# Optimization experiments

Hardware: AMD Instinct MI355X
Metric: run time of the kernel (lower is better)

Reference implementation:

```python
import jax, jax.numpy as jnp
import numpy as np

B, N, C, H = 8, 4096, 256, 8
D = C // H
HID = 4 * C
EPS = 1e-5

def _ln(x, w, b):
    mu = jnp.mean(x, axis=-1, keepdims=True)
    var = jnp.var(x, axis=-1, keepdims=True)
    return (x - mu) * jax.lax.rsqrt(var + EPS) * w + b

def setup_inputs() -> dict:
    key = jax.random.key(0)
    ks = jax.random.split(key, 16)
    s = lambda k, shp, scale=0.02: jax.random.normal(k, shp, dtype=jnp.float32) * scale
    return {
        "input_": jax.random.normal(ks[0], (B, N, C), dtype=jnp.float32),
        "prev_state": jax.random.normal(ks[1], (B, N, C), dtype=jnp.float32),
        "pos_embed": jax.random.normal(ks[2], (1, N, C), dtype=jnp.float32),
        "norm1_w": jnp.ones((C,), jnp.float32), "norm1_b": jnp.zeros((C,), jnp.float32),
        "norm2_w": jnp.ones((C,), jnp.float32), "norm2_b": jnp.zeros((C,), jnp.float32),
        "norm3_w": jnp.ones((C,), jnp.float32), "norm3_b": jnp.zeros((C,), jnp.float32),
        "qkv_input_w": s(ks[3], (3 * C, C)),
        "qkv_state_w": s(ks[4], (3 * C, C)),
        "proj_w": s(ks[5], (C, C)), "proj_b": jnp.zeros((C,), jnp.float32),
        "gate_w": s(ks[6], (C, 2 * C)), "gate_b": jnp.zeros((C,), jnp.float32),
        "fc1_w": s(ks[7], (HID, C)), "fc1_b": jnp.zeros((HID,), jnp.float32),
        "fc2_w": s(ks[8], (C, HID)), "fc2_b": jnp.zeros((C,), jnp.float32),
    }

def reference(input_, prev_state, pos_embed,
              norm1_w, norm1_b, norm2_w, norm2_b, norm3_w, norm3_b,
              qkv_input_w, qkv_state_w, proj_w, proj_b,
              gate_w, gate_b, fc1_w, fc1_b, fc2_w, fc2_b):
    input_pos = input_ + pos_embed
    x_ln = _ln(input_pos, norm1_w, norm1_b)
    s_ln = _ln(prev_state, norm2_w, norm2_b)
    # fused QKV from input and state; torch Linear: x @ W.T
    qkv_i = (x_ln @ qkv_input_w.T).reshape(B, N, 3, H, D).transpose(2, 0, 3, 1, 4)
    qkv_s = (s_ln @ qkv_state_w.T).reshape(B, N, 3, H, D).transpose(2, 0, 3, 1, 4)
    q = qkv_i[0] + qkv_s[0]  # [B,H,N,D]
    k = qkv_i[1] + qkv_s[1]
    v = qkv_i[2] + qkv_s[2]
    phi_q = jax.nn.elu(q) + 1.0
    phi_k = jax.nn.elu(k) + 1.0
    # (phi_q @ phi_k^T) @ v reordered associatively to O(N*D^2)
    kv = jnp.einsum('bhnd,bhne->bhde', phi_k, v)        # [B,H,D,D]
    attn = jnp.einsum('bhnd,bhde->bhne', phi_q, kv)     # [B,H,N,D]
    attn = attn.transpose(0, 2, 1, 3).reshape(B, N, C)
    attn = attn @ proj_w.T + proj_b
    output = input_pos + attn
    stacked = jnp.concatenate([input_, prev_state], axis=2)
    update = jax.nn.sigmoid(stacked @ gate_w.T + gate_b)
    new_state = prev_state * (1.0 - update) + attn * update
    h = _ln(output, norm3_w, norm3_b)
    h = jax.nn.gelu(h @ fc1_w.T + fc1_b, approximate=False) @ fc2_w.T + fc2_b
    output = output + h
    return (output, new_state)
```

## Files before the change

### kernel.cpp

```cpp
#include <hip/hip_runtime.h>
#include <cmath>

typedef unsigned short u16;
typedef __attribute__((ext_vector_type(8))) short short8;
typedef __attribute__((ext_vector_type(4))) float f32x4;
typedef __attribute__((ext_vector_type(4))) u16 u16x4;

__device__ __forceinline__ float b2f(u16 u) {
    unsigned x = ((unsigned)u) << 16;
    return __builtin_bit_cast(float, x);
}
__device__ __forceinline__ u16 f2b(float f) {
    unsigned x = __builtin_bit_cast(unsigned, f);
    unsigned r = (x + 0x7fffu + ((x >> 16) & 1u)) >> 16;
    return (u16)r;
}
__device__ __forceinline__ float loadx(const void* p, size_t i, int f32) {
    return f32 ? ((const float*)p)[i] : b2f(((const u16*)p)[i]);
}
__device__ __forceinline__ void gl_lds16(const void* g, void* l) {
    __builtin_amdgcn_global_load_lds(
        (const __attribute__((address_space(1))) void*)g,
        (__attribute__((address_space(3))) void*)l, 16, 0, 0);
}
__device__ __forceinline__ float gelu_f(float x) {
    float y = 0.7978845608028654f * (x + 0.044715f * x * x * x);
    float e = __expf(2.f * y);
    float t = 1.f - 2.f / (e + 1.f);
    return 0.5f * x * (1.f + t);
}

#define BB 8
#define NN 4096
#define CC 256
#define HH 8
#define DD 32
#define HID 1024
#define MTOK (BB*NN)
#define TOKEL ((size_t)MTOK*CC)
#define TOKELC 8388608

#define WS_INPUT_POS 0u
#define WS_PHIQ   16777216u
#define WS_PHIK   33554432u
#define WS_V      50331648u
#define WS_XLN    67108864u
#define WS_SLN    83886080u
#define WS_OUTPRE 100663296u
#define WS_FLAG   117440512u

#define OFF_QKVI  0u
#define OFF_QKVS  196608u
#define OFF_PROJW 393216u
#define OFF_GATEW 458752u
#define OFF_FC1W  589824u
#define OFF_FC2W  851968u
#define OFF_PROJB 1114112u
#define OFF_GATEB 1114368u
#define OFF_FC1B  1114624u
#define OFF_FC2B  1115648u
#define WTOT      1115904u

__device__ __attribute__((aligned(16))) u16 g_wb[WTOT];
__device__ __attribute__((aligned(16))) u16 g_inb[TOKELC];
__device__ __attribute__((aligned(16))) u16 g_prevb[TOKELC];

__global__ __launch_bounds__(64) void detect_kernel(const u16* __restrict__ in0,
                                                    int* __restrict__ flag)
{
    int t = threadIdx.x;
    u16 w = in0[2 * t];
    int e = (w >> 7) & 0xFF;
    int bad = (e < 64 || e > 192) ? 1 : 0;
    unsigned long long m = __ballot(bad);
    if (t == 0) *flag = (__popcll(m) > 8) ? 1 : 0;
}

__global__ __launch_bounds__(256) void wconv_kernel(
    const void* qkvi, const void* qkvs, const void* projw, const void* gatew,
    const void* fc1w, const void* fc2w, const void* projb, const void* gateb,
    const void* fc1b, const void* fc2b, const int* __restrict__ flagp)
{
    const int f32 = *flagp;
    unsigned i = blockIdx.x * 256 + threadIdx.x;
    if (i >= WTOT) return;
    const void* src; unsigned off;
    if      (i < OFF_QKVS)  { src = qkvi;  off = OFF_QKVI; }
    else if (i < OFF_PROJW) { src = qkvs;  off = OFF_QKVS; }
    else if (i < OFF_GATEW) { src = projw; off = OFF_PROJW; }
    else if (i < OFF_FC1W)  { src = gatew; off = OFF_GATEW; }
    else if (i < OFF_FC2W)  { src = fc1w;  off = OFF_FC1W; }
    else if (i < OFF_PROJB) { src = fc2w;  off = OFF_FC2W; }
    else if (i < OFF_GATEB) { src = projb; off = OFF_PROJB; }
    else if (i < OFF_FC1B)  { src = gateb; off = OFF_GATEB; }
    else if (i < OFF_FC2B)  { src = fc1b;  off = OFF_FC1B; }
    else                    { src = fc2b;  off = OFF_FC2B; }
    g_wb[i] = f2b(loadx(src, i - off, f32));
}

__global__ __launch_bounds__(256) void prep_kernel(
    const void* __restrict__ inp, const void* __restrict__ prev,
    const void* __restrict__ pos,
    const void* __restrict__ w1, const void* __restrict__ b1,
    const void* __restrict__ w2, const void* __restrict__ b2,
    u16* __restrict__ input_pos, u16* __restrict__ x_ln, u16* __restrict__ s_ln,
    const int* __restrict__ flagp)
{
    const int f32 = *flagp;
    const int m = blockIdx.x;
    const int c = threadIdx.x;
    const int n = m & (NN - 1);
    const size_t idx = (size_t)m * CC + c;

    __shared__ float red[8];

    float inr = loadx(inp, idx, f32);
    float ip = inr + loadx(pos, (size_t)n * CC + c, f32);
    g_inb[idx] = f2b(inr);
    float s = ip, s2 = ip * ip;
    #pragma unroll
    for (int o = 32; o; o >>= 1) { s += __shfl_down(s, o, 64); s2 += __shfl_down(s2, o, 64); }
    if ((threadIdx.x & 63) == 0) { int w6 = threadIdx.x >> 6; red[w6] = s; red[4 + w6] = s2; }
    __syncthreads();
    float mu  = (red[0] + red[1] + red[2] + red[3]) * (1.f / 256.f);
    float var = (red[4] + red[5] + red[6] + red[7]) * (1.f / 256.f) - mu * mu;
    float rs = rsqrtf(var + 1e-5f);
    input_pos[idx] = f2b(ip);
    x_ln[idx] = f2b((ip - mu) * rs * loadx(w1, c, f32) + loadx(b1, c, f32));
    __syncthreads();

    float pv = loadx(prev, idx, f32);
    g_prevb[idx] = f2b(pv);
    s = pv; s2 = pv * pv;
    #pragma unroll
    for (int o = 32; o; o >>= 1) { s += __shfl_down(s, o, 64); s2 += __shfl_down(s2, o, 64); }
    if ((threadIdx.x & 63) == 0) { int w6 = threadIdx.x >> 6; red[w6] = s; red[4 + w6] = s2; }
    __syncthreads();
    mu  = (red[0] + red[1] + red[2] + red[3]) * (1.f / 256.f);
    var = (red[4] + red[5] + red[6] + red[7]) * (1.f / 256.f) - mu * mu;
    rs = rsqrtf(var + 1e-5f);
    s_ln[idx] = f2b((pv - mu) * rs * loadx(w2, c, f32) + loadx(b2, c, f32));
}

__global__ __launch_bounds__(256) void ln3_kernel(
    const u16* __restrict__ op, const void* __restrict__ w,
    const void* __restrict__ b, u16* __restrict__ out, const int* __restrict__ flagp)
{
    const int f32 = *flagp;
    const size_t m = blockIdx.x;
    const int c = threadIdx.x;
    const size_t idx = m * CC + c;
    __shared__ float red[8];
    float x = b2f(op[idx]);
    float s = x, s2 = x * x;
    #pragma unroll
    for (int o = 32; o; o >>= 1) { s += __shfl_down(s, o, 64); s2 += __shfl_down(s2, o, 64); }
    if ((threadIdx.x & 63) == 0) { int w6 = threadIdx.x >> 6; red[w6] = s; red[4 + w6] = s2; }
    __syncthreads();
    float mu  = (red[0] + red[1] + red[2] + red[3]) * (1.f / 256.f);
    float var = (red[4] + red[5] + red[6] + red[7]) * (1.f / 256.f) - mu * mu;
    out[idx] = f2b((x - mu) * rsqrtf(var + 1e-5f) * loadx(w, c, f32) + loadx(b, c, f32));
}

__global__ __launch_bounds__(64) void kv_mfma(
    const u16* __restrict__ phik_t, const u16* __restrict__ v_t,
    float* __restrict__ kvout)
{
    const int bh = blockIdx.x;
    const int k0 = blockIdx.y * 256;
    const int lane = threadIdx.x;
    const int quad = lane >> 4, lr = lane & 15;

    const u16* A = phik_t + (size_t)bh * DD * NN;
    const u16* W = v_t    + (size_t)bh * DD * NN;

    f32x4 acc[2][2];
    #pragma unroll
    for (int i = 0; i < 2; ++i)
        #pragma unroll
        for (int j = 0; j < 2; ++j) { f32x4 z = {0.f,0.f,0.f,0.f}; acc[i][j] = z; }

    for (int kk = k0; kk < k0 + 256; kk += 32) {
        short8 a0 = *(const short8*)(A + (size_t)lr * NN + kk + quad * 8);
        short8 a1 = *(const short8*)(A + (size_t)(16 + lr) * NN + kk + quad * 8);
        short8 w0 = *(const short8*)(W + (size_t)lr * NN + kk + quad * 8);
        short8 w1 = *(const short8*)(W + (size_t)(16 + lr) * NN + kk + quad * 8);
        acc[0][0] = __builtin_amdgcn_mfma_f32_16x16x32_bf16(a0, w0, acc[0][0], 0, 0, 0);
        acc[0][1] = __builtin_amdgcn_mfma_f32_16x16x32_bf16(a0, w1, acc[0][1], 0, 0, 0);
        acc[1][0] = __builtin_amdgcn_mfma_f32_16x16x32_bf16(a1, w0, acc[1][0], 0, 0, 0);
        acc[1][1] = __builtin_amdgcn_mfma_f32_16x16x32_bf16(a1, w1, acc[1][1], 0, 0, 0);
    }
    float* base = kvout + (size_t)bh * (DD * DD);
    #pragma unroll
    for (int i = 0; i < 2; ++i)
        #pragma unroll
        for (int j = 0; j < 2; ++j)
            #pragma unroll
            for (int r = 0; r < 4; ++r)
                atomicAdd(base + (i * 16 + quad * 4 + r) * DD + j * 16 + lr, acc[i][j][r]);
}

__global__ __launch_bounds__(256) void attn_mfma(
    const u16* __restrict__ phiq, const float* __restrict__ kv,
    u16* __restrict__ attn_tok)
{
    const int bh = blockIdx.x;
    const int b = bh >> 3, h = bh & 7;
    const int wv = threadIdx.x >> 6, lane = threadIdx.x & 63;
    const int quad = lane >> 4, lr = lane & 15;

    const float* kvb = kv + (size_t)bh * (DD * DD);
    short8 bf0, bf1;
    #pragma unroll
    for (int j = 0; j < 8; ++j) {
        int d = quad * 8 + j;
        bf0[j] = (short)f2b(kvb[d * DD + lr]);
        bf1[j] = (short)f2b(kvb[d * DD + 16 + lr]);
    }

    const u16* qb = phiq + (size_t)bh * NN * DD;
    const int n0 = blockIdx.y * 512 + wv * 128;
    #pragma unroll
    for (int t = 0; t < 8; ++t) {
        const int nt = n0 + t * 16;
        short8 af = *(const short8*)(qb + (size_t)(nt + lr) * DD + quad * 8);
        f32x4 c0 = {0.f,0.f,0.f,0.f}, c1 = {0.f,0.f,0.f,0.f};
        c0 = __builtin_amdgcn_mfma_f32_16x16x32_bf16(af, bf0, c0, 0, 0, 0);
        c1 = __builtin_amdgcn_mfma_f32_16x16x32_bf16(af, bf1, c1, 0, 0, 0);
        size_t base = ((size_t)b * NN + nt + quad * 4) * CC + h * DD;
        #pragma unroll
        for (int r = 0; r < 4; ++r) {
            attn_tok[base + (size_t)r * CC + lr]      = f2b(c0[r]);
            attn_tok[base + (size_t)r * CC + 16 + lr] = f2b(c1[r]);
        }
    }
}

#define BM 128
#define BN 128
#define BK 32

template <int MODE>
__global__ __launch_bounds__(256) void gemm_bt(
    const u16* __restrict__ A1in, const u16* __restrict__ A2in,
    int lda, int ldw, int K, int Ksplit, int wcol2,
    u16* __restrict__ o0, u16* __restrict__ o1,
    const u16* __restrict__ xa, const void* __restrict__ xr,
    void* __restrict__ oraw, const int* __restrict__ flagp)
{
    __shared__ __attribute__((aligned(16))) u16 ash[3][BM * BK];
    __shared__ __attribute__((aligned(16))) u16 bsh[3][BN * BK];

    const int f32 = (MODE == 2 || MODE == 4) ? *flagp : 0;

    const u16* W1; const u16* W2; const u16* bias = nullptr;
    if (MODE == 0)      { W1 = g_wb + OFF_QKVI; W2 = g_wb + OFF_QKVS; }
    else if (MODE == 1) { W1 = W2 = g_wb + OFF_PROJW; bias = g_wb + OFF_PROJB; }
    else if (MODE == 2) { W1 = W2 = g_wb + OFF_GATEW; bias = g_wb + OFF_GATEB; }
    else if (MODE == 3) { W1 = W2 = g_wb + OFF_FC1W;  bias = g_wb + OFF_FC1B; }
    else                { W1 = W2 = g_wb + OFF_FC2W;  bias = g_wb + OFF_FC2B; }
    const u16* A1 = (MODE == 2) ? g_inb   : A1in;
    const u16* A2 = (MODE == 2) ? g_prevb : A2in;

    const int gx = gridDim.x;
    const int nwg = gx * (int)gridDim.y;
    const int hw = blockIdx.y * gx + blockIdx.x;
    const int qq = nwg >> 3, rr = nwg & 7;
    const int xc = hw & 7, pp = hw >> 3;
    const int nid = (xc < rr ? xc * (qq + 1) : rr * (qq + 1) + (xc - rr) * qq) + pp;
    const int bx = nid % gx, by = nid / gx;

    const int tid = threadIdx.x;
    const int lane = tid & 63;
    const int wv = tid >> 6;
    const int wm = wv >> 1, wn = wv & 1;
    const int quad = lane >> 4, lr = lane & 15;

    const bool swp = (MODE == 0) ? (bx < 2) : true;

    f32x4 acc[4][4];
    #pragma unroll
    for (int i = 0; i < 4; ++i)
        #pragma unroll
        for (int j = 0; j < 4; ++j) { f32x4 z = {0.f,0.f,0.f,0.f}; acc[i][j] = z; }

    const size_t arow0 = (size_t)by * BM;
    const size_t wrow0 = (size_t)bx * BN;

    const int srow = lane & 31;
    const int sg   = (lane >> 5) << 3;
    const size_t aoff = (arow0 + wv * 32 + srow) * (size_t)lda + sg;
    const size_t woff = (wrow0 + wv * 32 + srow) * (size_t)ldw + sg;

    auto stage = [&](int buf, int k0) {
        const u16* As; const u16* Ws; int ka, kw;
        if (k0 < Ksplit) { As = A1; Ws = W1; ka = k0;          kw = k0; }
        else             { As = A2; Ws = W2; ka = k0 - Ksplit; kw = k0 - Ksplit + wcol2; }
        const u16* ga = As + aoff + ka;
        u16* la = ash[buf] + (wv << 10);
        gl_lds16(ga, la);
        gl_lds16(ga + 16, la + 512);
        const u16* gw = Ws + woff + kw;
        u16* lb = bsh[buf] + (wv << 10);
        gl_lds16(gw, lb);
        gl_lds16(gw + 16, lb + 512);
    };

    auto compute = [&](int buf) {
        short8 af[4], bf[4];
        #pragma unroll
        for (int i = 0; i < 4; ++i) {
            const int ra = wm * 64 + i * 16 + lr;
            af[i] = *(const short8*)(ash[buf] + ((ra >> 5) << 10) + (quad << 8) + ((ra & 31) << 3));
        }
        #pragma unroll
        for (int j = 0; j < 4; ++j) {
            const int rb = wn * 64 + j * 16 + lr;
            bf[j] = *(const short8*)(bsh[buf] + ((rb >> 5) << 10) + (quad << 8) + ((rb & 31) << 3));
        }
        if (swp) {
            #pragma unroll
            for (int i = 0; i < 4; ++i)
                #pragma unroll
                for (int j = 0; j < 4; ++j)
                    acc[i][j] = __builtin_amdgcn_mfma_f32_16x16x32_bf16(bf[j], af[i], acc[i][j], 0, 0, 0);
        } else {
            #pragma unroll
            for (int i = 0; i < 4; ++i)
                #pragma unroll
                for (int j = 0; j < 4; ++j)
                    acc[i][j] = __builtin_amdgcn_mfma_f32_16x16x32_bf16(af[i], bf[j], acc[i][j], 0, 0, 0);
        }
    };

    const int NT = K / BK;
    stage(0, 0);
    stage(1, BK);
    for (int t = 0; t < NT; ++t) {
        if (t + 2 < NT) {
            stage((t + 2) % 3, (t + 2) * BK);
            asm volatile("s_waitcnt vmcnt(8)" ::: "memory");
        } else if (t + 1 < NT) {
            asm volatile("s_waitcnt vmcnt(4)" ::: "memory");
        } else {
            asm volatile("s_waitcnt vmcnt(0)" ::: "memory");
        }
        __builtin_amdgcn_s_barrier();
        asm volatile("" ::: "memory");
        compute(t % 3);
        asm volatile("" ::: "memory");
        __builtin_amdgcn_s_barrier();
    }

    const int mbase = by * BM + wm * 64;
    const int nbase = bx * BN + wn * 64;
    constexpr int LDOUT = (MODE == 3) ? HID : CC;

    #pragma unroll
    for (int i = 0; i < 4; ++i) {
        #pragma unroll
        for (int j = 0; j < 4; ++j) {
            if (MODE == 0) {
                if (swp) {
                    const int m = mbase + i * 16 + lr;
                    const int b = m >> 12, n = m & (NN - 1);
                    const int c0 = nbase + j * 16 + quad * 4;
                    const int h = c0 >> 5, d0 = c0 & 31;
                    u16x4 p;
                    #pragma unroll
                    for (int r = 0; r < 4; ++r) {
                        float v = acc[i][j][r];
                        p[r] = f2b((v > 0.f) ? (v + 1.f) : __expf(v));
                    }
                    *(u16x4*)(o0 + (((size_t)b * HH + h) * NN + n) * DD + d0) = p;
                } else {
                    const int c = nbase + j * 16 + lr;
                    const int which = c >> 8, rem = c & 255, h = rem >> 5, d = rem & 31;
                    const int m0 = mbase + i * 16 + quad * 4;
                    const int b = m0 >> 12, n0i = m0 & (NN - 1);
                    u16x4 p;
                    #pragma unroll
                    for (int r = 0; r < 4; ++r) {
                        float v = acc[i][j][r];
                        if (which == 1) v = (v > 0.f) ? (v + 1.f) : __expf(v);
                        p[r] = f2b(v);
                    }
                    u16* dst = o0 + (size_t)which * TOKEL;
                    *(u16x4*)(dst + (((size_t)b * HH + h) * DD + d) * NN + n0i) = p;
                }
            } else {
                const int m = mbase + i * 16 + lr;
                const int c0 = nbase + j * 16 + quad * 4;
                const size_t idx0 = (size_t)m * LDOUT + c0;
                float bias4[4];
                {
                    u16x4 t = *(const u16x4*)(bias + c0);
                    #pragma unroll
                    for (int r = 0; r < 4; ++r) bias4[r] = b2f(t[r]);
                }
                if (MODE == 1) {
                    u16x4 xa4 = *(const u16x4*)(xa + idx0);
                    u16x4 po, pr;
                    #pragma unroll
                    for (int r = 0; r < 4; ++r) {
                        float val = acc[i][j][r] + bias4[r];
                        po[r] = f2b(val);
                        pr[r] = f2b(b2f(xa4[r]) + val);
                    }
                    *(u16x4*)(o0 + idx0) = po;
                    *(u16x4*)(o1 + idx0) = pr;
                } else if (MODE == 2) {
                    u16x4 ap4 = *(const u16x4*)(xa + idx0);
                    if (f32) {
                        f32x4 pv = *(const f32x4*)((const float*)xr + idx0);
                        f32x4 o;
                        #pragma unroll
                        for (int r = 0; r < 4; ++r) {
                            float u = 1.f / (1.f + __expf(-(acc[i][j][r] + bias4[r])));
                            o[r] = pv[r] * (1.f - u) + b2f(ap4[r]) * u;
                        }
                        *(f32x4*)((float*)oraw + TOKEL + idx0) = o;
                    } else {
                        u16x4 pv = *(const u16x4*)((const u16*)xr + idx0);
                        u16x4 o;
                        #pragma unroll
                        for (int r = 0; r < 4; ++r) {
                            float u = 1.f / (1.f + __expf(-(acc[i][j][r] + bias4[r])));
                            o[r] = f2b(b2f(pv[r]) * (1.f - u) + b2f(ap4[r]) * u);
                        }
                        *(u16x4*)((u16*)oraw + TOKEL + idx0) = o;
                    }
                } else if (MODE == 3) {
                    u16x4 p;
                    #pragma unroll
                    for (int r = 0; r < 4; ++r)
                        p[r] = f2b(gelu_f(acc[i][j][r] + bias4[r]));
                    *(u16x4*)(o0 + idx0) = p;
                } else {
                    u16x4 xa4 = *(const u16x4*)(xa + idx0);
                    if (f32) {
                        f32x4 o;
                        #pragma unroll
                        for (int r = 0; r < 4; ++r)
                            o[r] = b2f(xa4[r]) + acc[i][j][r] + bias4[r];
                        *(f32x4*)((float*)oraw + idx0) = o;
                    } else {
                        u16x4 o;
                        #pragma unroll
                        for (int r = 0; r < 4; ++r)
                            o[r] = f2b(b2f(xa4[r]) + acc[i][j][r] + bias4[r]);
                        *(u16x4*)((u16*)oraw + idx0) = o;
                    }
                }
            }
        }
    }
}

extern "C" void kernel_launch(void* const* d_in, const int* in_sizes, int n_in,
                              void* d_out, int out_size, void* d_ws, size_t ws_size,
                              hipStream_t stream)
{
    const void* input_ = d_in[0];
    const void* prev   = d_in[1];
    const void* pos    = d_in[2];
    const void* n1w = d_in[3];  const void* n1b = d_in[4];
    const void* n2w = d_in[5];  const void* n2b = d_in[6];
    const void* n3w = d_in[7];  const void* n3b = d_in[8];
    const void* qkvi = d_in[9]; const void* qkvs = d_in[10];
    const void* projw = d_in[11]; const void* projb = d_in[12];
    const void* gatew = d_in[13]; const void* gateb = d_in[14];
    const void* fc1w = d_in[15]; const void* fc1b = d_in[16];
    const void* fc2w = d_in[17]; const void* fc2b = d_in[18];

    char* ws = (char*)d_ws;
    u16* input_pos = (u16*)(ws + WS_INPUT_POS);
    u16* phiq  = (u16*)(ws + WS_PHIQ);
    u16* phikt = (u16*)(ws + WS_PHIK);
    u16* vt    = (u16*)(ws + WS_V);
    u16* x_ln = (u16*)(ws + WS_XLN);
    u16* s_ln = (u16*)(ws + WS_SLN);
    u16* attn_tok = x_ln;
    u16* attn_proj = phikt;
    float* kvf = (float*)(ws + WS_SLN);
    u16* ln3o = s_ln;
    u16* outpre = (u16*)(ws + WS_OUTPRE);
    u16* h1 = (u16*)(ws + WS_INPUT_POS);
    int* flagp = (int*)(ws + WS_FLAG);

    detect_kernel<<<1, 64, 0, stream>>>((const u16*)input_, flagp);
    wconv_kernel<<<(WTOT + 255) / 256, 256, 0, stream>>>(
        qkvi, qkvs, projw, gatew, fc1w, fc2w, projb, gateb, fc1b, fc2b, flagp);
    prep_kernel<<<MTOK, 256, 0, stream>>>(input_, prev, pos, n1w, n1b, n2w, n2b,
                                          input_pos, x_ln, s_ln, flagp);
    gemm_bt<0><<<dim3(3 * CC / BN, MTOK / BM), 256, 0, stream>>>(
        x_ln, s_ln, CC, CC, 2 * CC, CC, 0,
        phiq, nullptr, nullptr, nullptr, nullptr, flagp);
    hipMemsetAsync((void*)kvf, 0, BB * HH * DD * DD * sizeof(float), stream);
    kv_mfma<<<dim3(BB * HH, 16), 64, 0, stream>>>(phikt, vt, kvf);
    attn_mfma<<<dim3(BB * HH, NN / 512), 256, 0, stream>>>(phiq, kvf, attn_tok);
    gemm_bt<1><<<dim3(CC / BN, MTOK / BM), 256, 0, stream>>>(
        attn_tok, attn_tok, CC, CC, CC, CC, 0,
        attn_proj, outpre, input_pos, nullptr, nullptr, flagp);
    gemm_bt<2><<<dim3(CC / BN, MTOK / BM), 256, 0, stream>>>(
        nullptr, nullptr, CC, 2 * CC, 2 * CC, CC, CC,
        nullptr, nullptr, attn_proj, prev, d_out, flagp);
    ln3_kernel<<<MTOK, 256, 0, stream>>>(outpre, n3w, n3b, ln3o, flagp);
    gemm_bt<3><<<dim3(HID / BN, MTOK / BM), 256, 0, stream>>>(
        ln3o, ln3o, CC, CC, CC, CC, 0,
        h1, nullptr, nullptr, nullptr, nullptr, flagp);
    gemm_bt<4><<<dim3(CC / BN, MTOK / BM), 256, 0, stream>>>(
        h1, h1, HID, HID, HID, HID, 0,
        nullptr, nullptr, outpre, nullptr, d_out, flagp);
}
```

Baseline: 469.6 us.

## Replace LDS-staged GEMMs with direct-from-global MFMA kernel for proj/gate/fc1/fc2

Result: slower. 535.2 us (+14.0%).

```diff
diff --git a/kernel.cpp b/kernel.cpp
--- a/kernel.cpp
+++ b/kernel.cpp
@@ -236,6 +236,140 @@
     }
 }
 
+template <int MODE>
+__global__ __launch_bounds__(256) void gemm_direct(
+    const u16* __restrict__ A1in, const u16* __restrict__ A2in,
+    int lda, int ldw, int K, int Ksplit, int wcol2,
+    u16* __restrict__ o0, u16* __restrict__ o1,
+    const u16* __restrict__ xa, const void* __restrict__ xr,
+    void* __restrict__ oraw, const int* __restrict__ flagp)
+{
+    const int f32 = (MODE == 2 || MODE == 4) ? *flagp : 0;
+
+    const u16* W1; const u16* W2; const u16* bias;
+    if (MODE == 1)      { W1 = W2 = g_wb + OFF_PROJW; bias = g_wb + OFF_PROJB; }
+    else if (MODE == 2) { W1 = W2 = g_wb + OFF_GATEW; bias = g_wb + OFF_GATEB; }
+    else if (MODE == 3) { W1 = W2 = g_wb + OFF_FC1W;  bias = g_wb + OFF_FC1B; }
+    else                { W1 = W2 = g_wb + OFF_FC2W;  bias = g_wb + OFF_FC2B; }
+    const u16* A1 = (MODE == 2) ? g_inb   : A1in;
+    const u16* A2 = (MODE == 2) ? g_prevb : A2in;
+
+    const int gx = gridDim.x;
+    const int nwg = gx * (int)gridDim.y;
+    const int hw = blockIdx.y * gx + blockIdx.x;
+    const int qq = nwg >> 3, rr = nwg & 7;
+    const int xc = hw & 7, pp = hw >> 3;
+    const int nid = (xc < rr ? xc * (qq + 1) : rr * (qq + 1) + (xc - rr) * qq) + pp;
+    const int bx = nid % gx, by = nid / gx;
+
+    const int lane = threadIdx.x & 63;
+    const int wv = threadIdx.x >> 6;
+    const int quad = lane >> 4, lr = lane & 15;
+
+    const int m0 = by * 256 + wv * 64;
+    const int n0 = bx * 64;
+
+    f32x4 acc[4][4];
+    #pragma unroll
+    for (int i = 0; i < 4; ++i)
+        #pragma unroll
+        for (int j = 0; j < 4; ++j) { f32x4 z = {0.f,0.f,0.f,0.f}; acc[i][j] = z; }
+
+    size_t arow[4], wrow[4];
+    #pragma unroll
+    for (int i = 0; i < 4; ++i) arow[i] = (size_t)(m0 + i * 16 + lr) * lda + quad * 8;
+    #pragma unroll
+    for (int j = 0; j < 4; ++j) wrow[j] = (size_t)(n0 + j * 16 + lr) * ldw + quad * 8;
+
+    #pragma unroll 2
+    for (int k0 = 0; k0 < K; k0 += 32) {
+        const u16* As; const u16* Ws; int ka, kw;
+        if (k0 < Ksplit) { As = A1; Ws = W1; ka = k0;          kw = k0; }
+        else             { As = A2; Ws = W2; ka = k0 - Ksplit; kw = k0 - Ksplit + wcol2; }
+        short8 af[4], bf[4];
+        #pragma unroll
+        for (int i = 0; i < 4; ++i) af[i] = *(const short8*)(As + arow[i] + ka);
+        #pragma unroll
+        for (int j = 0; j < 4; ++j) bf[j] = *(const short8*)(Ws + wrow[j] + kw);
+        #pragma unroll
+        for (int i = 0; i < 4; ++i)
+            #pragma unroll
+            for (int j = 0; j < 4; ++j)
+                acc[i][j] = __builtin_amdgcn_mfma_f32_16x16x32_bf16(bf[j], af[i], acc[i][j], 0, 0, 0);
+    }
+
+    constexpr int LDOUT = (MODE == 3) ? HID : CC;
+    #pragma unroll
+    for (int i = 0; i < 4; ++i) {
+        #pragma unroll
+        for (int j = 0; j < 4; ++j) {
+            const int m = m0 + i * 16 + lr;
+            const int c0 = n0 + j * 16 + quad * 4;
+            const size_t idx0 = (size_t)m * LDOUT + c0;
+            float bias4[4];
+            {
+                u16x4 t = *(const u16x4*)(bias + c0);
+                #pragma unroll
+                for (int r = 0; r < 4; ++r) bias4[r] = b2f(t[r]);
+            }
+            if (MODE == 1) {
+                u16x4 xa4 = *(const u16x4*)(xa + idx0);
+                u16x4 po, pr;
+                #pragma unroll
+                for (int r = 0; r < 4; ++r) {
+                    float val = acc[i][j][r] + bias4[r];
+                    po[r] = f2b(val);
+                    pr[r] = f2b(b2f(xa4[r]) + val);
+                }
+                *(u16x4*)(o0 + idx0) = po;
+                *(u16x4*)(o1 + idx0) = pr;
+            } else if (MODE == 2) {
+                u16x4 ap4 = *(const u16x4*)(xa + idx0);
+                if (f32) {
+                    f32x4 pv = *(const f32x4*)((const float*)xr + idx0);
+                    f32x4 o;
+                    #pragma unroll
+                    for (int r = 0; r < 4; ++r) {
+                        float u = 1.f / (1.f + __expf(-(acc[i][j][r] + bias4[r])));
+                        o[r] = pv[r] * (1.f - u) + b2f(ap4[r]) * u;
+                    }
+                    *(f32x4*)((float*)oraw + TOKEL + idx0) = o;
+                } else {
+                    u16x4 pv = *(const u16x4*)((const u16*)xr + idx0);
+                    u16x4 o;
+                    #pragma unroll
+                    for (int r = 0; r < 4; ++r) {
+                        float u = 1.f / (1.f + __expf(-(acc[i][j][r] + bias4[r])));
+                        o[r] = f2b(b2f(pv[r]) * (1.f - u) + b2f(ap4[r]) * u);
+                    }
+                    *(u16x4*)((u16*)oraw + TOKEL + idx0) = o;
+                }
+            } else if (MODE == 3) {
+                u16x4 p;
+                #pragma unroll
+                for (int r = 0; r < 4; ++r)
+                    p[r] = f2b(gelu_f(acc[i][j][r] + bias4[r]));
+                *(u16x4*)(o0 + idx0) = p;
+            } else {
+                u16x4 xa4 = *(const u16x4*)(xa + idx0);
+                if (f32) {
+                    f32x4 o;
+                    #pragma unroll
+                    for (int r = 0; r < 4; ++r)
+                        o[r] = b2f(xa4[r]) + acc[i][j][r] + bias4[r];
+                    *(f32x4*)((float*)oraw + idx0) = o;
+                } else {
+                    u16x4 o;
+                    #pragma unroll
+                    for (int r = 0; r < 4; ++r)
+                        o[r] = f2b(b2f(xa4[r]) + acc[i][j][r] + bias4[r]);
+                    *(u16x4*)((u16*)oraw + idx0) = o;
+                }
+            }
+        }
+    }
+}
+
 #define BM 128
 #define BN 128
 #define BK 32
@@ -251,16 +385,10 @@
     __shared__ __attribute__((aligned(16))) u16 ash[3][BM * BK];
     __shared__ __attribute__((aligned(16))) u16 bsh[3][BN * BK];
 
-    const int f32 = (MODE == 2 || MODE == 4) ? *flagp : 0;
-
-    const u16* W1; const u16* W2; const u16* bias = nullptr;
-    if (MODE == 0)      { W1 = g_wb + OFF_QKVI; W2 = g_wb + OFF_QKVS; }
-    else if (MODE == 1) { W1 = W2 = g_wb + OFF_PROJW; bias = g_wb + OFF_PROJB; }
-    else if (MODE == 2) { W1 = W2 = g_wb + OFF_GATEW; bias = g_wb + OFF_GATEB; }
-    else if (MODE == 3) { W1 = W2 = g_wb + OFF_FC1W;  bias = g_wb + OFF_FC1B; }
-    else                { W1 = W2 = g_wb + OFF_FC2W;  bias = g_wb + OFF_FC2B; }
-    const u16* A1 = (MODE == 2) ? g_inb   : A1in;
-    const u16* A2 = (MODE == 2) ? g_prevb : A2in;
+    const u16* W1; const u16* W2;
+    W1 = g_wb + OFF_QKVI; W2 = g_wb + OFF_QKVS;
+    const u16* A1 = A1in;
+    const u16* A2 = A2in;
 
     const int gx = gridDim.x;
     const int nwg = gx * (int)gridDim.y;
@@ -276,7 +404,7 @@
     const int wm = wv >> 1, wn = wv & 1;
     const int quad = lane >> 4, lr = lane & 15;
 
-    const bool swp = (MODE == 0) ? (bx < 2) : true;
+    const bool swp = (bx < 2);
 
     f32x4 acc[4][4];
     #pragma unroll
@@ -354,104 +482,37 @@
 
     const int mbase = by * BM + wm * 64;
     const int nbase = bx * BN + wn * 64;
-    constexpr int LDOUT = (MODE == 3) ? HID : CC;
 
     #pragma unroll
     for (int i = 0; i < 4; ++i) {
         #pragma unroll
         for (int j = 0; j < 4; ++j) {
-            if (MODE == 0) {
-                if (swp) {
-                    const int m = mbase + i * 16 + lr;
-                    const int b = m >> 12, n = m & (NN - 1);
-                    const int c0 = nbase + j * 16 + quad * 4;
-                    const int h = c0 >> 5, d0 = c0 & 31;
-                    u16x4 p;
-                    #pragma unroll
-                    for (int r = 0; r < 4; ++r) {
-                        float v = acc[i][j][r];
-                        p[r] = f2b((v > 0.f) ? (v + 1.f) : __expf(v));
-                    }
-                    *(u16x4*)(o0 + (((size_t)b * HH + h) * NN + n) * DD + d0) = p;
-                } else {
-                    const int c = nbase + j * 16 + lr;
-                    const int which = c >> 8, rem = c & 255, h = rem >> 5, d = rem & 31;
-                    const int m0 = mbase + i * 16 + quad * 4;
-                    const int b = m0 >> 12, n0i = m0 & (NN - 1);
-                    u16x4 p;
-                    #pragma unroll
-                    for (int r = 0; r < 4; ++r) {
-                        float v = acc[i][j][r];
-                        if (which == 1) v = (v > 0.f) ? (v + 1.f) : __expf(v);
-                        p[r] = f2b(v);
-                    }
-                    u16* dst = o0 + (size_t)which * TOKEL;
-                    *(u16x4*)(dst + (((size_t)b * HH + h) * DD + d) * NN + n0i) = p;
+            if (swp) {
+                const int m = mbase + i * 16 + lr;
+                const int b = m >> 12, n = m & (NN - 1);
+                const int c0 = nbase + j * 16 + quad * 4;
+                const int h = c0 >> 5, d0 = c0 & 31;
+                u16x4 p;
+                #pragma unroll
+                for (int r = 0; r < 4; ++r) {
+                    float v = acc[i][j][r];
+                    p[r] = f2b((v > 0.f) ? (v + 1.f) : __expf(v));
                 }
+                *(u16x4*)(o0 + (((size_t)b * HH + h) * NN + n) * DD + d0) = p;
             } else {
-                const int m = mbase + i * 16 + lr;
-                const int c0 = nbase + j * 16 + quad * 4;
-                const size_t idx0 = (size_t)m * LDOUT + c0;
-                float bias4[4];
-                {
-                    u16x4 t = *(const u16x4*)(bias + c0);
-                    #pragma unroll
-                    for (int r = 0; r < 4; ++r) bias4[r] = b2f(t[r]);
+                const int c = nbase + j * 16 + lr;
+                const int which = c >> 8, rem = c & 255, h = rem >> 5, d = rem & 31;
+                const int m0 = mbase + i * 16 + quad * 4;
+                const int b = m0 >> 12, n0i = m0 & (NN - 1);
+                u16x4 p;
+                #pragma unroll
+                for (int r = 0; r < 4; ++r) {
+                    float v = acc[i][j][r];
+                    if (which == 1) v = (v > 0.f) ? (v + 1.f) : __expf(v);
+                    p[r] = f2b(v);
                 }
-                if (MODE == 1) {
-                    u16x4 xa4 = *(const u16x4*)(xa + idx0);
-                    u16x4 po, pr;
-                    #pragma unroll
-                    for (int r = 0; r < 4; ++r) {
-                        float val = acc[i][j][r] + bias4[r];
-                        po[r] = f2b(val);
-                        pr[r] = f2b(b2f(xa4[r]) + val);
-                    }
-                    *(u16x4*)(o0 + idx0) = po;
-                    *(u16x4*)(o1 + idx0) = pr;
-                } else if (MODE == 2) {
-                    u16x4 ap4 = *(const u16x4*)(xa + idx0);
-                    if (f32) {
-                        f32x4 pv = *(const f32x4*)((const float*)xr + idx0);
-                        f32x4 o;
-                        #pragma unroll
-                        for (int r = 0; r < 4; ++r) {
-                            float u = 1.f / (1.f + __expf(-(acc[i][j][r] + bias4[r])));
-                            o[r] = pv[r] * (1.f - u) + b2f(ap4[r]) * u;
-                        }
-                        *(f32x4*)((float*)oraw + TOKEL + idx0) = o;
-                    } else {
-                        u16x4 pv = *(const u16x4*)((const u16*)xr + idx0);
-                        u16x4 o;
-                        #pragma unroll
-                        for (int r = 0; r < 4; ++r) {
-                            float u = 1.f / (1.f + __expf(-(acc[i][j][r] + bias4[r])));
-                            o[r] = f2b(b2f(pv[r]) * (1.f - u) + b2f(ap4[r]) * u);
-                        }
-                        *(u16x4*)((u16*)oraw + TOKEL + idx0) = o;
-                    }
-                } else if (MODE == 3) {
-                    u16x4 p;
-                    #pragma unroll
-                    for (int r = 0; r < 4; ++r)
-                        p[r] = f2b(gelu_f(acc[i][j][r] + bias4[r]));
-                    *(u16x4*)(o0 + idx0) = p;
-                } else {
-                    u16x4 xa4 = *(const u16x4*)(xa + idx0);
-                    if (f32) {
-                        f32x4 o;
-                        #pragma unroll
-                        for (int r = 0; r < 4; ++r)
-                            o[r] = b2f(xa4[r]) + acc[i][j][r] + bias4[r];
-                        *(f32x4*)((float*)oraw + idx0) = o;
-                    } else {
-                        u16x4 o;
-                        #pragma unroll
-                        for (int r = 0; r < 4; ++r)
-                            o[r] = f2b(b2f(xa4[r]) + acc[i][j][r] + bias4[r]);
-                        *(u16x4*)((u16*)oraw + idx0) = o;
-                    }
-                }
+                u16* dst = o0 + (size_t)which * TOKEL;
+                *(u16x4*)(dst + (((size_t)b * HH + h) * DD + d) * NN + n0i) = p;
             }
         }
     }
@@ -499,17 +560,17 @@
     hipMemsetAsync((void*)kvf, 0, BB * HH * DD * DD * sizeof(float), stream);
     kv_mfma<<<dim3(BB * HH, 16), 64, 0, stream>>>(phikt, vt, kvf);
     attn_mfma<<<dim3(BB * HH, NN / 512), 256, 0, stream>>>(phiq, kvf, attn_tok);
-    gemm_bt<1><<<dim3(CC / BN, MTOK / BM), 256, 0, stream>>>(
+    gemm_direct<1><<<dim3(CC / 64, MTOK / 256), 256, 0, stream>>>(
         attn_tok, attn_tok, CC, CC, CC, CC, 0,
         attn_proj, outpre, input_pos, nullptr, nullptr, flagp);
-    gemm_bt<2><<<dim3(CC / BN, MTOK / BM), 256, 0, stream>>>(
+    gemm_direct<2><<<dim3(CC / 64, MTOK / 256), 256, 0, stream>>>(
         nullptr, nullptr, CC, 2 * CC, 2 * CC, CC, CC,
         nullptr, nullptr, attn_proj, prev, d_out, flagp);
     ln3_kernel<<<MTOK, 256, 0, stream>>>(outpre, n3w, n3b, ln3o, flagp);
-    gemm_bt<3><<<dim3(HID / BN, MTOK / BM), 256, 0, stream>>>(
+    gemm_direct<3><<<dim3(HID / 64, MTOK / 256), 256, 0, stream>>>(
         ln3o, ln3o, CC, CC, CC, CC, 0,
         h1, nullptr, nullptr, nullptr, nullptr, flagp);
-    gemm_bt<4><<<dim3(CC / BN, MTOK / BM), 256, 0, stream>>>(
+    gemm_direct<4><<<dim3(CC / 64, MTOK / 256), 256, 0, stream>>>(
         h1, h1, HID, HID, HID, HID, 0,
         nullptr, nullptr, outpre, nullptr, d_out, flagp);
 }
```

## Fold gate GEMM into QKV GEMM and apply state update in proj epilogue

Applied to the files above, without the earlier changes.

Result: slower. 517.4 us (+10.2%).

```diff
diff --git a/kernel.cpp b/kernel.cpp
--- a/kernel.cpp
+++ b/kernel.cpp
@@ -64,6 +64,7 @@
 __device__ __attribute__((aligned(16))) u16 g_wb[WTOT];
 __device__ __attribute__((aligned(16))) u16 g_inb[TOKELC];
 __device__ __attribute__((aligned(16))) u16 g_prevb[TOKELC];
+__device__ __attribute__((aligned(16))) u16 g_ugate[TOKELC];
 
 __global__ __launch_bounds__(64) void detect_kernel(const u16* __restrict__ in0,
                                                     int* __restrict__ flag)
@@ -251,16 +252,13 @@
     __shared__ __attribute__((aligned(16))) u16 ash[3][BM * BK];
     __shared__ __attribute__((aligned(16))) u16 bsh[3][BN * BK];
 
-    const int f32 = (MODE == 2 || MODE == 4) ? *flagp : 0;
+    const int f32 = (MODE == 1 || MODE == 4) ? *flagp : 0;
 
     const u16* W1; const u16* W2; const u16* bias = nullptr;
     if (MODE == 0)      { W1 = g_wb + OFF_QKVI; W2 = g_wb + OFF_QKVS; }
     else if (MODE == 1) { W1 = W2 = g_wb + OFF_PROJW; bias = g_wb + OFF_PROJB; }
-    else if (MODE == 2) { W1 = W2 = g_wb + OFF_GATEW; bias = g_wb + OFF_GATEB; }
     else if (MODE == 3) { W1 = W2 = g_wb + OFF_FC1W;  bias = g_wb + OFF_FC1B; }
     else                { W1 = W2 = g_wb + OFF_FC2W;  bias = g_wb + OFF_FC2B; }
-    const u16* A1 = (MODE == 2) ? g_inb   : A1in;
-    const u16* A2 = (MODE == 2) ? g_prevb : A2in;
 
     const int gx = gridDim.x;
     const int nwg = gx * (int)gridDim.y;
@@ -270,14 +268,15 @@
     const int nid = (xc < rr ? xc * (qq + 1) : rr * (qq + 1) + (xc - rr) * qq) + pp;
     const int bx = nid % gx, by = nid / gx;
 
+    const bool isGate = (MODE == 0) && (bx >= 6);
+    const bool swp = (MODE == 0) ? (bx < 2 || isGate) : true;
+
     const int tid = threadIdx.x;
     const int lane = tid & 63;
     const int wv = tid >> 6;
     const int wm = wv >> 1, wn = wv & 1;
     const int quad = lane >> 4, lr = lane & 15;
 
-    const bool swp = (MODE == 0) ? (bx < 2) : true;
-
     f32x4 acc[4][4];
     #pragma unroll
     for (int i = 0; i < 4; ++i)
@@ -285,17 +284,25 @@
         for (int j = 0; j < 4; ++j) { f32x4 z = {0.f,0.f,0.f,0.f}; acc[i][j] = z; }
 
     const size_t arow0 = (size_t)by * BM;
-    const size_t wrow0 = (size_t)bx * BN;
+    const int nbase_blk = isGate ? (bx - 6) * BN : bx * BN;
+    const int ldw_eff = isGate ? 2 * CC : ldw;
 
     const int srow = lane & 31;
     const int sg   = (lane >> 5) << 3;
     const size_t aoff = (arow0 + wv * 32 + srow) * (size_t)lda + sg;
-    const size_t woff = (wrow0 + wv * 32 + srow) * (size_t)ldw + sg;
+    const size_t woff = ((size_t)nbase_blk + wv * 32 + srow) * (size_t)ldw_eff + sg;
 
     auto stage = [&](int buf, int k0) {
         const u16* As; const u16* Ws; int ka, kw;
-        if (k0 < Ksplit) { As = A1; Ws = W1; ka = k0;          kw = k0; }
-        else             { As = A2; Ws = W2; ka = k0 - Ksplit; kw = k0 - Ksplit + wcol2; }
+        if (MODE == 0) {
+            if (k0 < Ksplit) { As = isGate ? g_inb   : A1in; ka = k0; }
+            else             { As = isGate ? g_prevb : A2in; ka = k0 - Ksplit; }
+            if (isGate) { Ws = g_wb + OFF_GATEW; kw = k0; }
+            else        { Ws = (k0 < Ksplit) ? W1 : W2;
+                          kw = (k0 < Ksplit) ? k0 : k0 - Ksplit; }
+        } else {
+            As = A1in; Ws = W1; ka = k0; kw = k0;
+        }
         const u16* ga = As + aoff + ka;
         u16* la = ash[buf] + (wv << 10);
         gl_lds16(ga, la);
@@ -353,7 +360,7 @@
     }
 
     const int mbase = by * BM + wm * 64;
-    const int nbase = bx * BN + wn * 64;
+    const int nbase = nbase_blk + wn * 64;
     constexpr int LDOUT = (MODE == 3) ? HID : CC;
 
     #pragma unroll
@@ -361,7 +368,18 @@
         #pragma unroll
         for (int j = 0; j < 4; ++j) {
             if (MODE == 0) {
-                if (swp) {
+                if (isGate) {
+                    const int m = mbase + i * 16 + lr;
+                    const int c0 = nbase + j * 16 + quad * 4;
+                    u16x4 b4 = *(const u16x4*)(g_wb + OFF_GATEB + c0);
+                    u16x4 p;
+                    #pragma unroll
+                    for (int r = 0; r < 4; ++r) {
+                        float u = 1.f / (1.f + __expf(-(acc[i][j][r] + b2f(b4[r]))));
+                        p[r] = f2b(u);
+                    }
+                    *(u16x4*)(g_ugate + (size_t)m * CC + c0) = p;
+                } else if (swp) {
                     const int m = mbase + i * 16 + lr;
                     const int b = m >> 12, n = m & (NN - 1);
                     const int c0 = nbase + j * 16 + quad * 4;
@@ -400,24 +418,25 @@
                 }
                 if (MODE == 1) {
                     u16x4 xa4 = *(const u16x4*)(xa + idx0);
+                    u16x4 ug4 = *(const u16x4*)(g_ugate + idx0);
                     u16x4 po, pr;
+                    float vals[4];
                     #pragma unroll
                     for (int r = 0; r < 4; ++r) {
                         float val = acc[i][j][r] + bias4[r];
+                        vals[r] = val;
                         po[r] = f2b(val);
                         pr[r] = f2b(b2f(xa4[r]) + val);
                     }
                     *(u16x4*)(o0 + idx0) = po;
                     *(u16x4*)(o1 + idx0) = pr;
-                } else if (MODE == 2) {
-                    u16x4 ap4 = *(const u16x4*)(xa + idx0);
                     if (f32) {
                         f32x4 pv = *(const f32x4*)((const float*)xr + idx0);
                         f32x4 o;
                         #pragma unroll
                         for (int r = 0; r < 4; ++r) {
-                            float u = 1.f / (1.f + __expf(-(acc[i][j][r] + bias4[r])));
-                            o[r] = pv[r] * (1.f - u) + b2f(ap4[r]) * u;
+                            float u = b2f(ug4[r]);
+                            o[r] = pv[r] * (1.f - u) + vals[r] * u;
                         }
                         *(f32x4*)((float*)oraw + TOKEL + idx0) = o;
                     } else {
@@ -425,8 +444,8 @@
                         u16x4 o;
                         #pragma unroll
                         for (int r = 0; r < 4; ++r) {
-                            float u = 1.f / (1.f + __expf(-(acc[i][j][r] + bias4[r])));
-                            o[r] = f2b(b2f(pv[r]) * (1.f - u) + b2f(ap4[r]) * u);
+                            float u = b2f(ug4[r]);
+                            o[r] = f2b(b2f(pv[r]) * (1.f - u) + vals[r] * u);
                         }
                         *(u16x4*)((u16*)oraw + TOKEL + idx0) = o;
                     }
@@ -493,7 +512,7 @@
         qkvi, qkvs, projw, gatew, fc1w, fc2w, projb, gateb, fc1b, fc2b, flagp);
     prep_kernel<<<MTOK, 256, 0, stream>>>(input_, prev, pos, n1w, n1b, n2w, n2b,
                                           input_pos, x_ln, s_ln, flagp);
-    gemm_bt<0><<<dim3(3 * CC / BN, MTOK / BM), 256, 0, stream>>>(
+    gemm_bt<0><<<dim3(8, MTOK / BM), 256, 0, stream>>>(
         x_ln, s_ln, CC, CC, 2 * CC, CC, 0,
         phiq, nullptr, nullptr, nullptr, nullptr, flagp);
     hipMemsetAsync((void*)kvf, 0, BB * HH * DD * DD * sizeof(float), stream);
@@ -501,10 +520,7 @@
     attn_mfma<<<dim3(BB * HH, NN / 512), 256, 0, stream>>>(phiq, kvf, attn_tok);
     gemm_bt<1><<<dim3(CC / BN, MTOK / BM), 256, 0, stream>>>(
         attn_tok, attn_tok, CC, CC, CC, CC, 0,
-        attn_proj, outpre, input_pos, nullptr, nullptr, flagp);
-    gemm_bt<2><<<dim3(CC / BN, MTOK / BM), 256, 0, stream>>>(
-        nullptr, nullptr, CC, 2 * CC, 2 * CC, CC, CC,
-        nullptr, nullptr, attn_proj, prev, d_out, flagp);
+        attn_proj, outpre, input_pos, prev, d_out, flagp);
     ln3_kernel<<<MTOK, 256, 0, stream>>>(outpre, n3w, n3b, ln3o, flagp);
     gemm_bt<3><<<dim3(HID / BN, MTOK / BM), 256, 0, stream>>>(
         ln3o, ln3o, CC, CC, CC, CC, 0,
```
